# Optimization experiments

Hardware: AMD Instinct MI355X
Metric: run time of the kernel (lower is better)

## Reference

```python
import jax, jax.numpy as jnp
import numpy as np

GRAY_LEVELS = 16
DISTANCE = 1
ANGLES = (0, 45, 90, 135)


def _glcm_entropy(img):
    """img: [H, W] float in [0,1). Returns scalar entropy of the pooled GLCM."""
    L = GRAY_LEVELS
    d = DISTANCE
    # torch does (img * (L-1)).to(uint8): truncation toward zero for non-negative inputs
    q = (img * (L - 1)).astype(jnp.int32)  # [H, W], values in [0, L-1]
    counts = jnp.zeros((L * L,), jnp.float32)
    for angle in ANGLES:  # small fixed loop over 4 angles
        if angle == 0:
            s = jnp.roll(q, d, axis=1)
        elif angle == 45:
            s = jnp.roll(q, (d, -d), axis=(0, 1))
        elif angle == 90:
            s = jnp.roll(q, d, axis=0)
        elif angle == 135:
            s = jnp.roll(q, (d, d), axis=(0, 1))
        else:
            raise ValueError('Unsupported angle.')
        # fused scatter-add histogram over joint (i, j) bins, replaces L^2 mask-sums
        idx = (q * L + s).reshape(-1)  # [H*W]
        counts = counts.at[idx].add(1.0)
    glcm = counts / counts.sum()
    return -jnp.sum(glcm * jnp.log(glcm + 1e-10))


def setup_inputs() -> dict:
    key = jax.random.key(0)
    x = jax.random.uniform(key, (8, 16, 512, 512), dtype=jnp.float32)
    return {"x": x}


def reference(x):
    B, C, H, W = x.shape
    ent = jax.vmap(_glcm_entropy)(x.reshape(B * C, H, W))  # [B*C]
    # each (b,c) slice of the output is filled with that image's scalar entropy
    return jnp.broadcast_to(ent.reshape(B, C, 1, 1), (B, C, H, W))
```

## Files before the change

### kernel.cpp

```cpp
#include <hip/hip_runtime.h>
#include <math.h>

#define IMG_H    512
#define IMG_W    512
#define IMG_HW   (IMG_H * IMG_W)
#define N_IMG    128
#define NBINS    256
#define FILL_PER_IMG 16

typedef float f32x4 __attribute__((ext_vector_type(4)));

template<int NSTRIPS>
__global__ __launch_bounds__(256) void glcm_hist_kernel(
    const float* __restrict__ x, unsigned int* __restrict__ partial) {

    constexpr int ROWS  = IMG_H / NSTRIPS;
    constexpr int ITERS = ROWS / 2;

    __shared__ unsigned int lh[8][NBINS];
    const int tid   = threadIdx.x;
    const int bid   = blockIdx.x;
    const int img   = bid / NSTRIPS;
    const int strip = bid % NSTRIPS;

    #pragma unroll
    for (int i = tid; i < 8 * NBINS; i += 256) ((unsigned int*)lh)[i] = 0u;
    __syncthreads();

    const float* __restrict__ base = x + (size_t)img * IMG_HW;
    unsigned int* mh = lh[tid >> 5];

    const int half = tid >> 7;
    const int jj   = (tid & 127) << 2;
    const int jm1  = (jj + IMG_W - 1) & (IMG_W - 1);
    const int jp4  = (jj + 4) & (IMG_W - 1);
    const int rowBase = strip * ROWS;

    float4 c4, u4; float cm1, um1, up4;
    {
        const int r  = rowBase + half;
        const int ru = (r + IMG_H - 1) & (IMG_H - 1);
        c4  = *reinterpret_cast<const float4*>(base + (size_t)r  * IMG_W + jj);
        u4  = *reinterpret_cast<const float4*>(base + (size_t)ru * IMG_W + jj);
        cm1 = base[(size_t)r  * IMG_W + jm1];
        um1 = base[(size_t)ru * IMG_W + jm1];
        up4 = base[(size_t)ru * IMG_W + jp4];
    }

    for (int it = 0; it < ITERS; ++it) {
        float4 nc4, nu4; float ncm1, num1, nup4;
        if (it + 1 < ITERS) {
            const int r  = rowBase + (it + 1) * 2 + half;
            const int ru = (r + IMG_H - 1) & (IMG_H - 1);
            nc4  = *reinterpret_cast<const float4*>(base + (size_t)r  * IMG_W + jj);
            nu4  = *reinterpret_cast<const float4*>(base + (size_t)ru * IMG_W + jj);
            ncm1 = base[(size_t)r  * IMG_W + jm1];
            num1 = base[(size_t)ru * IMG_W + jm1];
            nup4 = base[(size_t)ru * IMG_W + jp4];
        }

        int qc[5];
        int qu[6];
        qc[0] = (int)(cm1 * 15.0f);
        qc[1] = (int)(c4.x * 15.0f); qc[2] = (int)(c4.y * 15.0f);
        qc[3] = (int)(c4.z * 15.0f); qc[4] = (int)(c4.w * 15.0f);
        qu[0] = (int)(um1 * 15.0f);
        qu[1] = (int)(u4.x * 15.0f); qu[2] = (int)(u4.y * 15.0f);
        qu[3] = (int)(u4.z * 15.0f); qu[4] = (int)(u4.w * 15.0f);
        qu[5] = (int)(up4 * 15.0f);

        #pragma unroll
        for (int k = 0; k < 4; ++k) {
            const int q = qc[k + 1] << 4;
            atomicAdd(&mh[q + qc[k]],     1u);
            atomicAdd(&mh[q + qu[k + 2]], 1u);
            atomicAdd(&mh[q + qu[k + 1]], 1u);
            atomicAdd(&mh[q + qu[k]],     1u);
        }

        c4 = nc4; u4 = nu4; cm1 = ncm1; um1 = num1; up4 = nup4;
    }

    __syncthreads();
    unsigned int total = 0;
    #pragma unroll
    for (int h = 0; h < 8; ++h) total += lh[h][tid];
    partial[(size_t)(img * NSTRIPS + strip) * NBINS + tid] = total;
}

template<int NSTRIPS>
__global__ __launch_bounds__(256) void glcm_entfill_kernel(
    const unsigned int* __restrict__ partial, float* __restrict__ out) {

    __shared__ float psum[4];
    __shared__ float ent_s;
    const int tid = threadIdx.x;
    const int bid = blockIdx.x;
    const int img = bid >> 4;
    const int sub = bid & 15;

    unsigned int c = 0;
    #pragma unroll
    for (int s = 0; s < NSTRIPS; ++s)
        c += partial[(size_t)(img * NSTRIPS + s) * NBINS + tid];

    const float p = (float)c * (1.0f / 1048576.0f);
    float t = p * logf(p + 1e-10f);
    #pragma unroll
    for (int off = 32; off > 0; off >>= 1) t += __shfl_down(t, off, 64);
    if ((tid & 63) == 0) psum[tid >> 6] = t;
    __syncthreads();
    if (tid == 0) ent_s = -(psum[0] + psum[1] + psum[2] + psum[3]);
    __syncthreads();

    const float e = ent_s;
    const f32x4 v = {e, e, e, e};
    f32x4* ob = reinterpret_cast<f32x4*>(out) +
                (size_t)img * (IMG_HW / 4) + (size_t)sub * (IMG_HW / 4 / FILL_PER_IMG);
    #pragma unroll
    for (int i = tid; i < IMG_HW / 4 / FILL_PER_IMG; i += 256)
        __builtin_nontemporal_store(v, ob + i);
}

extern "C" void kernel_launch(void* const* d_in, const int* in_sizes, int n_in,
                              void* d_out, int out_size, void* d_ws, size_t ws_size,
                              hipStream_t stream) {
    const float* x = (const float*)d_in[0];
    float* out = (float*)d_out;
    unsigned int* partial = (unsigned int*)d_ws;

    if (ws_size >= (size_t)N_IMG * 16 * NBINS * sizeof(unsigned int)) {
        glcm_hist_kernel<16><<<N_IMG * 16, 256, 0, stream>>>(x, partial);
        glcm_entfill_kernel<16><<<N_IMG * FILL_PER_IMG, 256, 0, stream>>>(partial, out);
    } else {
        glcm_hist_kernel<8><<<N_IMG * 8, 256, 0, stream>>>(x, partial);
        glcm_entfill_kernel<8><<<N_IMG * FILL_PER_IMG, 256, 0, stream>>>(partial, out);
    }
}
```

Baseline: 67.96 us.

## Use per-lane packed 16-bit LDS histograms to eliminate atomic contention

Replaces eight shared 256-bin histograms per block with a private histogram per wave lane, packing two 16-bit bins per 32-bit word so each lane's atomics hit its own bank. This targets LDS atomic conflicts and bank conflicts from random bin collisions. The final reduction sums 64 lane copies with rotated indexing before writing partials. It raises LDS use to 32 KB per block, which can reduce occupancy, and fixes the strip count at 8, dropping the 16-strip path.

```diff
diff --git a/kernel.cpp b/kernel.cpp
--- a/kernel.cpp
+++ b/kernel.cpp
@@ -5,30 +5,30 @@
 #define IMG_W    512
 #define IMG_HW   (IMG_H * IMG_W)
 #define N_IMG    128
+#define NSTRIPS  8
 #define NBINS    256
 #define FILL_PER_IMG 16
 
 typedef float f32x4 __attribute__((ext_vector_type(4)));
 
-template<int NSTRIPS>
 __global__ __launch_bounds__(256) void glcm_hist_kernel(
     const float* __restrict__ x, unsigned int* __restrict__ partial) {
 
     constexpr int ROWS  = IMG_H / NSTRIPS;
     constexpr int ITERS = ROWS / 2;
 
-    __shared__ unsigned int lh[8][NBINS];
+    __shared__ unsigned int lh[128 * 64];
     const int tid   = threadIdx.x;
+    const int lane  = tid & 63;
     const int bid   = blockIdx.x;
-    const int img   = bid / NSTRIPS;
-    const int strip = bid % NSTRIPS;
+    const int img   = bid >> 3;
+    const int strip = bid & 7;
 
     #pragma unroll
-    for (int i = tid; i < 8 * NBINS; i += 256) ((unsigned int*)lh)[i] = 0u;
+    for (int i = tid; i < 128 * 64; i += 256) lh[i] = 0u;
     __syncthreads();
 
     const float* __restrict__ base = x + (size_t)img * IMG_HW;
-    unsigned int* mh = lh[tid >> 5];
 
     const int half = tid >> 7;
     const int jj   = (tid & 127) << 2;
@@ -71,24 +71,41 @@
 
         #pragma unroll
         for (int k = 0; k < 4; ++k) {
-            const int q = qc[k + 1] << 4;
-            atomicAdd(&mh[q + qc[k]],     1u);
-            atomicAdd(&mh[q + qu[k + 2]], 1u);
-            atomicAdd(&mh[q + qu[k + 1]], 1u);
-            atomicAdd(&mh[q + qu[k]],     1u);
+            const int rb = (qc[k + 1] << 9) + lane;
+            const int s0 = qc[k];
+            const int s1 = qu[k + 2];
+            const int s2 = qu[k + 1];
+            const int s3 = qu[k];
+            atomicAdd(&lh[rb + ((s0 >> 1) << 6)], 1u << ((s0 & 1) << 4));
+            atomicAdd(&lh[rb + ((s1 >> 1) << 6)], 1u << ((s1 & 1) << 4));
+            atomicAdd(&lh[rb + ((s2 >> 1) << 6)], 1u << ((s2 & 1) << 4));
+            atomicAdd(&lh[rb + ((s3 >> 1) << 6)], 1u << ((s3 & 1) << 4));
         }
 
         c4 = nc4; u4 = nu4; cm1 = ncm1; um1 = num1; up4 = nup4;
     }
 
     __syncthreads();
-    unsigned int total = 0;
+    const int p  = tid & 127;
+    const int hf = tid >> 7;
+    unsigned int slo = 0, shi = 0;
     #pragma unroll
-    for (int h = 0; h < 8; ++h) total += lh[h][tid];
-    partial[(size_t)(img * NSTRIPS + strip) * NBINS + tid] = total;
+    for (int i = 0; i < 32; ++i) {
+        const int l = (hf << 5) + ((p + i) & 31);
+        const unsigned int w = lh[(p << 6) + l];
+        slo += w & 0xffffu;
+        shi += w >> 16;
+    }
+    __syncthreads();
+    if (hf) { lh[p] = slo; lh[128 + p] = shi; }
+    __syncthreads();
+    if (!hf) {
+        const size_t ob = (size_t)(img * NSTRIPS + strip) * NBINS;
+        partial[ob + 2 * p]     = slo + lh[p];
+        partial[ob + 2 * p + 1] = shi + lh[128 + p];
+    }
 }
 
-template<int NSTRIPS>
 __global__ __launch_bounds__(256) void glcm_entfill_kernel(
     const unsigned int* __restrict__ partial, float* __restrict__ out) {
 
@@ -129,11 +146,6 @@
     float* out = (float*)d_out;
     unsigned int* partial = (unsigned int*)d_ws;
 
-    if (ws_size >= (size_t)N_IMG * 16 * NBINS * sizeof(unsigned int)) {
-        glcm_hist_kernel<16><<<N_IMG * 16, 256, 0, stream>>>(x, partial);
-        glcm_entfill_kernel<16><<<N_IMG * FILL_PER_IMG, 256, 0, stream>>>(partial, out);
-    } else {
-        glcm_hist_kernel<8><<<N_IMG * 8, 256, 0, stream>>>(x, partial);
-        glcm_entfill_kernel<8><<<N_IMG * FILL_PER_IMG, 256, 0, stream>>>(partial, out);
-    }
+    glcm_hist_kernel<<<N_IMG * NSTRIPS, 256, 0, stream>>>(x, partial);
+    glcm_entfill_kernel<<<N_IMG * FILL_PER_IMG, 256, 0, stream>>>(partial, out);
 }
```

New measurement: 64.14 us. -5.6%, faster.
